# Optimization experiments

Hardware: AMD Instinct MI355X
Metric: run time of the kernel (lower is better)

The kernel has to match this reference:

```python
import jax, jax.numpy as jnp
import numpy as np

DIM = 256      # slot / feature dim
S = 22         # num_slots (21 + 1 seg slot)
NAC = 20       # num_actor_class (slots truncated to this)
EPS = 1e-8     # slot-attention epsilon
LN_EPS = 1e-5  # torch LayerNorm default eps
RES = (4, 8, 24)  # (len_seg, H, W) grid for SoftPositionEmbed3D


def _ln(x, g, b):
    m = jnp.mean(x, -1, keepdims=True)
    v = jnp.var(x, -1, keepdims=True)
    return (x - m) * jax.lax.rsqrt(v + LN_EPS) * g + b


def _grid3d():
    # build_3d_grid: meshgrid of linspaces, concat [g, 1-g] -> (1, 4, 8, 24, 6)
    rs = [jnp.linspace(0.0, 1.0, r) for r in RES]
    g = jnp.stack(jnp.meshgrid(*rs, indexing='ij'), -1)
    return jnp.concatenate([g, 1.0 - g], -1)[None]


def setup_inputs() -> dict:
    key = jax.random.key(0)
    ks = iter(jax.random.split(key, 40))
    b, nf, h, w, d = 32, 16, 8, 24, DIM

    def lin(o, i):
        return (jax.random.normal(next(ks), (o, i)) / np.sqrt(i)).astype(jnp.float32)

    def vec(o):
        return jnp.zeros((o,), jnp.float32)

    inp = {}
    inp['inputs'] = jax.random.normal(next(ks), (b, nf, h, w, d), jnp.float32)
    inp['slots'] = jax.random.normal(next(ks), (1, S, d), jnp.float32)  # self.slots buffer
    inp['pe_w'] = lin(d, 6); inp['pe_b'] = vec(d)  # SoftPositionEmbed3D Linear(6, dim)
    for nm in ['LN', 'ni', 'ns', 'npf']:  # LN, norm_input, norm_slots, norm_pre_ff
        inp[nm + '_g'] = jnp.ones((d,), jnp.float32)
        inp[nm + '_b'] = vec(d)
    for nm in ['FC1', 'FC2', 'q', 'k', 'v', 'ff1', 'ff2']:
        inp[nm + '_w'] = lin(d, d)
        inp[nm + '_b'] = vec(d)
    inp['gru_wi'] = lin(3 * d, d); inp['gru_wh'] = lin(3 * d, d)
    inp['gru_bi'] = vec(3 * d);   inp['gru_bh'] = vec(3 * d)
    return inp


def reference(inputs, slots, pe_w, pe_b, LN_g, LN_b, ni_g, ni_b, ns_g, ns_b,
              npf_g, npf_b, FC1_w, FC1_b, FC2_w, FC2_b, q_w, q_b, k_w, k_b,
              v_w, v_b, ff1_w, ff1_b, ff2_w, ff2_b, gru_wi, gru_wh, gru_bi, gru_bh):
    b, nf, h, w, d = inputs.shape
    nwin = 7  # f in range(0, 13, 2)
    # slots are NOT carried across the frame loop in the original forward,
    # so the 7 windows are independent -> fold into batch.
    win = jnp.stack([inputs[:, f:f + 4] for f in range(0, 13, 2)], 0)  # (7,b,4,h,w,d)
    B = nwin * b
    pe = _grid3d() @ pe_w.T + pe_b  # (1,4,h,w,d)
    x = win.reshape(B, 4, h, w, d) + pe
    x = x.reshape(B, -1, d)  # n = 4*h*w tokens
    # LN -> FC1 -> relu -> FC2
    x = _ln(x, LN_g, LN_b)
    x = jax.nn.relu(x @ FC1_w.T + FC1_b) @ FC2_w.T + FC2_b
    # slot attention core
    xn = _ln(x, ni_g, ni_b)
    kk = xn @ k_w.T + k_b
    vv = xn @ v_w.T + v_b
    sl = jnp.broadcast_to(slots, (B, S, d))
    q = _ln(sl, ns_g, ns_b) @ q_w.T + q_b
    dots = jnp.einsum('bid,bjd->bij', q, kk) * (d ** -0.5)
    attn_ori = jax.nn.softmax(dots, axis=1) + EPS  # softmax over SLOT axis
    attn = attn_ori / jnp.sum(attn_ori, -1, keepdims=True)  # L1 renorm over tokens
    upd = jnp.einsum('bjd,bij->bid', vv, attn)
    # GRUCell(updates, slots_prev); torch gate order: r, z, n
    xg = upd.reshape(-1, d) @ gru_wi.T + gru_bi
    hprev = sl.reshape(-1, d)
    hg = hprev @ gru_wh.T + gru_bh
    ir, iz, in_ = jnp.split(xg, 3, -1)
    hr, hz, hn = jnp.split(hg, 3, -1)
    r = jax.nn.sigmoid(ir + hr)
    z = jax.nn.sigmoid(iz + hz)
    n = jnp.tanh(in_ + r * hn)
    hnew = (1.0 - z) * n + z * hprev
    so = hnew.reshape(B, S, d)[:, :NAC]
    # residual MLP
    so = so + jax.nn.relu(_ln(so, npf_g, npf_b) @ ff1_w.T + ff1_b) @ ff2_w.T + ff2_b
    slots_out = so.reshape(nwin, b, NAC, d).transpose(1, 0, 2, 3)      # (b,7,20,d)
    attns = attn_ori.reshape(nwin, b, S, -1).transpose(1, 0, 2, 3)     # (b,7,22,768)
    return slots_out, attns
```

## Files before the change

### kernel.cpp

```cpp
#include <hip/hip_runtime.h>

#define DEV static __device__ __forceinline__

namespace {
constexpr int D     = 256;
constexpr int SALL  = 22;
constexpr int NAC   = 20;
constexpr int NWIN  = 7;
constexpr int NB    = 32;
constexpr int NF    = 16;
constexpr int SPF   = 192;
constexpr int NTOK  = 768;
constexpr int BWIN  = 224;
constexpr int PARTS = 8;
constexpr int TPP   = 3;
constexpr float LNEPS = 1e-5f;
constexpr float EPS   = 1e-8f;
constexpr float SCL   = 0.0625f;

constexpr int OFF_PE   = 0;
constexpr int OFF_FC1T = OFF_PE   + 768 * 256;
constexpr int OFF_FC2T = OFF_FC1T + 256 * 256;
constexpr int OFF_VWT  = OFF_FC2T + 256 * 256;
constexpr int OFF_QWT  = OFF_VWT  + 256 * 256;
constexpr int OFF_FF1T = OFF_QWT  + 256 * 256;
constexpr int OFF_FF2T = OFF_FF1T + 256 * 256;
constexpr int OFF_GWIT = OFF_FF2T + 256 * 256;
constexpr int OFF_GWHT = OFF_GWIT + 256 * 768;
constexpr int OFF_Q    = OFF_GWHT + 256 * 768;
constexpr int OFF_QK2T = OFF_Q    + SALL * 256;
constexpr int OFF_QB   = OFF_QK2T + 256 * SALL;
constexpr int OFF_HG0  = OFF_QB   + 32;
constexpr int OFF_UPDP = OFF_HG0  + SALL * 768;
constexpr int OFF_RSP  = OFF_UPDP + BWIN * PARTS * NAC * 256;
}

DEV float4 ld4(const float* p) { return *(const float4*)p; }
DEV float sigm(float x) { return 1.f / (1.f + __expf(-x)); }

struct TPtrs {
    const float* src[8];
    float*       dst[8];
    int          osz[8];
};

__global__ void k_trans(TPtrs p) {
    __shared__ float t[32][33];
    const int bt = blockIdx.x;
    int m, tile;
    if (bt < 384) { m = bt >> 6; tile = bt & 63; }
    else          { m = 6 + (bt - 384) / 192; tile = (bt - 384) % 192; }
    const int O  = p.osz[m];
    const int rt = O >> 5;
    const int o0 = (tile % rt) * 32, i0 = (tile / rt) * 32;
    const int tx = threadIdx.x & 31, ty = threadIdx.x >> 5;
    const float* src = p.src[m];
    float*       dst = p.dst[m];
#pragma unroll
    for (int q = 0; q < 4; ++q) { int r = ty + q * 8; t[r][tx] = src[(o0 + r) * 256 + i0 + tx]; }
    __syncthreads();
#pragma unroll
    for (int q = 0; q < 4; ++q) { int r = ty + q * 8; dst[(i0 + r) * O + o0 + tx] = t[tx][r]; }
}

__global__ void k_pe(const float* __restrict__ pw, const float* __restrict__ pb,
                     float* __restrict__ pe) {
    const int p = blockIdx.x;
    const int fo = p / SPF, rem = p % SPF, hh = rem / 24, ww = rem % 24;
    const float g0 = fo * (1.f / 3.f), g1 = hh * (1.f / 7.f), g2 = ww * (1.f / 23.f);
    const float gg[6] = {g0, g1, g2, 1.f - g0, 1.f - g1, 1.f - g2};
    for (int d = threadIdx.x; d < 256; d += 64) {
        float acc = pb[d];
#pragma unroll
        for (int c = 0; c < 6; ++c) acc = fmaf(gg[c], pw[d * 6 + c], acc);
        pe[p * 256 + d] = acc;
    }
}

__global__ void k_q(const float* __restrict__ slots, const float* __restrict__ nsg,
                    const float* __restrict__ nsb, const float* __restrict__ qwT,
                    const float* __restrict__ qbias, const float* __restrict__ kb,
                    float* __restrict__ qout, float* __restrict__ qbout) {
    __shared__ float lnb[256];
    __shared__ float red[8];
    const int i = blockIdx.x, t = threadIdx.x, lane = t & 63, wvi = t >> 6;
    const float v = slots[i * 256 + t];
    float s1 = v, s2 = v * v;
#pragma unroll
    for (int m = 32; m; m >>= 1) { s1 += __shfl_xor(s1, m); s2 += __shfl_xor(s2, m); }
    if (lane == 0) { red[wvi] = s1; red[4 + wvi] = s2; }
    __syncthreads();
    const float fs = red[0] + red[1] + red[2] + red[3];
    const float fq = red[4] + red[5] + red[6] + red[7];
    const float mean = fs * (1.f / 256.f);
    const float var  = fq * (1.f / 256.f) - mean * mean;
    const float rstd = rsqrtf(var + LNEPS);
    lnb[t] = (v - mean) * rstd * nsg[t] + nsb[t];
    __syncthreads();
    float qv = qbias[t];
    for (int k = 0; k < 256; ++k) qv = fmaf(lnb[k], qwT[k * 256 + t], qv);
    qout[i * 256 + t] = qv;
    float pp = qv * kb[t];
#pragma unroll
    for (int m = 32; m; m >>= 1) pp += __shfl_xor(pp, m);
    __syncthreads();
    if (lane == 0) red[wvi] = pp;
    __syncthreads();
    if (t == 0) qbout[i] = red[0] + red[1] + red[2] + red[3];
}

__global__ void k_qk2(const float* __restrict__ qin, const float* __restrict__ kw,
                      float* __restrict__ qk2T) {
    __shared__ float qr[256];
    const int i = blockIdx.x, t = threadIdx.x;
    qr[t] = qin[i * 256 + t];
    __syncthreads();
    float acc = 0.f;
    for (int c = 0; c < 256; ++c) acc = fmaf(qr[c], kw[c * 256 + t], acc);
    qk2T[t * SALL + i] = acc;
}

__global__ void k_hg(const float* __restrict__ slots, const float* __restrict__ gwhT,
                     const float* __restrict__ gbh, float* __restrict__ hg0) {
    __shared__ float sr[256];
    const int i = blockIdx.x, t = threadIdx.x;
    sr[t] = slots[i * 256 + t];
    __syncthreads();
    float a0 = gbh[t], a1 = gbh[t + 256], a2 = gbh[t + 512];
    for (int k = 0; k < 256; ++k) {
        const float s = sr[k];
        a0 = fmaf(s, gwhT[k * 768 + t], a0);
        a1 = fmaf(s, gwhT[k * 768 + t + 256], a1);
        a2 = fmaf(s, gwhT[k * 768 + t + 512], a2);
    }
    hg0[i * 768 + t] = a0;
    hg0[i * 768 + t + 256] = a1;
    hg0[i * 768 + t + 512] = a2;
}

template <int MODE>
DEV void gemm_step(const float* __restrict__ srcL, float* __restrict__ dstL,
                   const float4* __restrict__ wT, const float4 bias,
                   const int lane, const int wv, const float4 gni, const float4 bni) {
    float acc[8][4];
#pragma unroll
    for (int j = 0; j < 8; ++j) {
        acc[j][0] = bias.x; acc[j][1] = bias.y; acc[j][2] = bias.z; acc[j][3] = bias.w;
    }
    const float* sp = srcL + (wv << 3) * 256;
    for (int k = 0; k < 256; k += 4) {
        const float4 w0 = wT[((k + 0) << 6) + lane];
        const float4 w1 = wT[((k + 1) << 6) + lane];
        const float4 w2 = wT[((k + 2) << 6) + lane];
        const float4 w3 = wT[((k + 3) << 6) + lane];
#pragma unroll
        for (int j = 0; j < 8; ++j) {
            const float4 x4 = *(const float4*)(sp + j * 256 + k);
            acc[j][0] = fmaf(x4.x, w0.x, acc[j][0]);
            acc[j][1] = fmaf(x4.x, w0.y, acc[j][1]);
            acc[j][2] = fmaf(x4.x, w0.z, acc[j][2]);
            acc[j][3] = fmaf(x4.x, w0.w, acc[j][3]);
            acc[j][0] = fmaf(x4.y, w1.x, acc[j][0]);
            acc[j][1] = fmaf(x4.y, w1.y, acc[j][1]);
            acc[j][2] = fmaf(x4.y, w1.z, acc[j][2]);
            acc[j][3] = fmaf(x4.y, w1.w, acc[j][3]);
            acc[j][0] = fmaf(x4.z, w2.x, acc[j][0]);
            acc[j][1] = fmaf(x4.z, w2.y, acc[j][1]);
            acc[j][2] = fmaf(x4.z, w2.z, acc[j][2]);
            acc[j][3] = fmaf(x4.z, w2.w, acc[j][3]);
            acc[j][0] = fmaf(x4.w, w3.x, acc[j][0]);
            acc[j][1] = fmaf(x4.w, w3.y, acc[j][1]);
            acc[j][2] = fmaf(x4.w, w3.z, acc[j][2]);
            acc[j][3] = fmaf(x4.w, w3.w, acc[j][3]);
        }
    }
#pragma unroll
    for (int j = 0; j < 8; ++j) {
        float4 o = {acc[j][0], acc[j][1], acc[j][2], acc[j][3]};
        if constexpr (MODE == 0) {
            o.x = fmaxf(o.x, 0.f); o.y = fmaxf(o.y, 0.f);
            o.z = fmaxf(o.z, 0.f); o.w = fmaxf(o.w, 0.f);
        } else if constexpr (MODE == 1) {
            float s  = o.x + o.y + o.z + o.w;
            float q2 = o.x * o.x + o.y * o.y + o.z * o.z + o.w * o.w;
#pragma unroll
            for (int m = 32; m; m >>= 1) { s += __shfl_xor(s, m); q2 += __shfl_xor(q2, m); }
            const float mean = s * (1.f / 256.f);
            const float var  = q2 * (1.f / 256.f) - mean * mean;
            const float rstd = rsqrtf(var + LNEPS);
            o.x = (o.x - mean) * rstd * gni.x + bni.x;
            o.y = (o.y - mean) * rstd * gni.y + bni.y;
            o.z = (o.z - mean) * rstd * gni.z + bni.z;
            o.w = (o.w - mean) * rstd * gni.w + bni.w;
        }
        ((float4*)dstL)[((wv << 3) + j) * 64 + lane] = o;
    }
}

__global__ __launch_bounds__(256, 2) void k_pass1(
    const float* __restrict__ gin, const float* __restrict__ ws_pe,
    const float4* __restrict__ fc1T, const float4* __restrict__ fc2T,
    const float4* __restrict__ vwT, const float* __restrict__ qk2T,
    const float* __restrict__ qb, const float* __restrict__ LNg,
    const float* __restrict__ LNb, const float* __restrict__ nig,
    const float* __restrict__ nib, const float* __restrict__ fc1b,
    const float* __restrict__ fc2b, const float* __restrict__ vb,
    float* __restrict__ attns, float* __restrict__ updp, float* __restrict__ rsp) {
    __shared__ __align__(16) float buf0[32 * 256];
    __shared__ __align__(16) float buf1[32 * 256];
    __shared__ __align__(16) float dotsL[SALL * 36];

    const int tid = threadIdx.x, lane = tid & 63, wv = tid >> 6;
    const int blk = blockIdx.x, bb = blk >> 3, part = blk & 7;
    const int wdx = bb >> 5, bi = bb & 31;
    const int c0 = lane << 2;

    const float4 gln = ld4(LNg + c0), bln = ld4(LNb + c0);
    const float4 gni = ld4(nig + c0), bni = ld4(nib + c0);
    const float4 b1 = ld4(fc1b + c0), b2 = ld4(fc2b + c0), bv = ld4(vb + c0);

    const int islot = tid & 31;
    const int iq = islot < SALL ? islot : SALL - 1;
    const float qbv = qb[iq];
    const int jg = tid >> 5;

    float upd[NAC];
#pragma unroll
    for (int i = 0; i < NAC; ++i) upd[i] = 0.f;
    float rsacc = 0.f;

    for (int tt = part * TPP; tt < part * TPP + TPP; ++tt) {
        const int fo = tt / 6, sp0 = (tt % 6) * 32;
        const float4* src = (const float4*)gin + ((bi * NF + 2 * wdx + fo) * SPF + sp0) * 64;
        const float4* pes = (const float4*)ws_pe + (fo * SPF + sp0) * 64;
#pragma unroll
        for (int ii = 0; ii < 8; ++ii) {
            float4 a = src[tid + 256 * ii];
            const float4 p = pes[tid + 256 * ii];
            a.x += p.x; a.y += p.y; a.z += p.z; a.w += p.w;
            float s  = a.x + a.y + a.z + a.w;
            float q2 = a.x * a.x + a.y * a.y + a.z * a.z + a.w * a.w;
#pragma unroll
            for (int m = 32; m; m >>= 1) { s += __shfl_xor(s, m); q2 += __shfl_xor(q2, m); }
            const float mean = s * (1.f / 256.f);
            const float var  = q2 * (1.f / 256.f) - mean * mean;
            const float rstd = rsqrtf(var + LNEPS);
            const int j = wv + (ii << 2);
            float4 o;
            o.x = (a.x - mean) * rstd * gln.x + bln.x;
            o.y = (a.y - mean) * rstd * gln.y + bln.y;
            o.z = (a.z - mean) * rstd * gln.z + bln.z;
            o.w = (a.w - mean) * rstd * gln.w + bln.w;
            ((float4*)buf0)[j * 64 + lane] = o;
        }
        __syncthreads();
        gemm_step<0>(buf0, buf1, fc1T, b1, lane, wv, gni, bni);
        __syncthreads();
        gemm_step<1>(buf1, buf0, fc2T, b2, lane, wv, gni, bni);
        __syncthreads();
        gemm_step<2>(buf0, buf1, vwT, bv, lane, wv, gni, bni);
        {
            float a0 = qbv, a1 = qbv, a2 = qbv, a3 = qbv;
            const float* x0 = buf0 + (jg * 4) * 256;
            for (int k = 0; k < 256; k += 4) {
                const float q0 = qk2T[(k + 0) * SALL + iq];
                const float q1 = qk2T[(k + 1) * SALL + iq];
                const float q2_ = qk2T[(k + 2) * SALL + iq];
                const float q3 = qk2T[(k + 3) * SALL + iq];
                const float4 x4a = *(const float4*)(x0 + 0 * 256 + k);
                const float4 x4b = *(const float4*)(x0 + 1 * 256 + k);
                const float4 x4c = *(const float4*)(x0 + 2 * 256 + k);
                const float4 x4d = *(const float4*)(x0 + 3 * 256 + k);
                a0 = fmaf(x4a.x, q0, fmaf(x4a.y, q1, fmaf(x4a.z, q2_, fmaf(x4a.w, q3, a0))));
                a1 = fmaf(x4b.x, q0, fmaf(x4b.y, q1, fmaf(x4b.z, q2_, fmaf(x4b.w, q3, a1))));
                a2 = fmaf(x4c.x, q0, fmaf(x4c.y, q1, fmaf(x4c.z, q2_, fmaf(x4c.w, q3, a2))));
                a3 = fmaf(x4d.x, q0, fmaf(x4d.y, q1, fmaf(x4d.z, q2_, fmaf(x4d.w, q3, a3))));
            }
            if (islot < SALL) {
                dotsL[islot * 36 + jg * 4 + 0] = a0 * SCL;
                dotsL[islot * 36 + jg * 4 + 1] = a1 * SCL;
                dotsL[islot * 36 + jg * 4 + 2] = a2 * SCL;
                dotsL[islot * 36 + jg * 4 + 3] = a3 * SCL;
            }
        }
        __syncthreads();
        if (tid < 32) {
            float dv[SALL];
            float mx = -1e30f;
#pragma unroll
            for (int i = 0; i < SALL; ++i) {
                dv[i] = dotsL[i * 36 + tid];
                mx = fmaxf(mx, dv[i]);
            }
            float sum = 0.f;
#pragma unroll
            for (int i = 0; i < SALL; ++i) { dv[i] = __expf(dv[i] - mx); sum += dv[i]; }
            const float inv = 1.f / sum;
#pragma unroll
            for (int i = 0; i < SALL; ++i) dotsL[i * 36 + tid] = dv[i] * inv + EPS;
        }
        __syncthreads();
        const int tok0 = tt * 32;
        float* ao = attns + bi * (NWIN * SALL * NTOK) + wdx * (SALL * NTOK) + tok0;
#pragma unroll
        for (int rep = 0; rep < 3; ++rep) {
            const int idx = tid + rep * 256;
            if (idx < SALL * 32) {
                const int i = idx >> 5, j = idx & 31;
                ao[i * NTOK + j] = dotsL[i * 36 + j];
            }
        }
        if (tid < NAC) {
            float s = 0.f;
#pragma unroll
            for (int j = 0; j < 32; ++j) s += dotsL[tid * 36 + j];
            rsacc += s;
        }
#pragma unroll
        for (int jq = 0; jq < 8; ++jq) {
            const float v0 = buf1[(jq * 4 + 0) * 256 + tid];
            const float v1 = buf1[(jq * 4 + 1) * 256 + tid];
            const float v2 = buf1[(jq * 4 + 2) * 256 + tid];
            const float v3 = buf1[(jq * 4 + 3) * 256 + tid];
#pragma unroll
            for (int i = 0; i < NAC; ++i) {
                const float4 a = *(const float4*)&dotsL[i * 36 + jq * 4];
                upd[i] = fmaf(a.x, v0, fmaf(a.y, v1, fmaf(a.z, v2, fmaf(a.w, v3, upd[i]))));
            }
        }
        __syncthreads();
    }
    float* up = updp + blk * (NAC * 256);
#pragma unroll
    for (int i = 0; i < NAC; ++i) up[i * 256 + tid] = upd[i];
    if (tid < NAC) rsp[blk * NAC + tid] = rsacc;
}

__global__ __launch_bounds__(256) void k_pass2(
    const float* __restrict__ updp, const float* __restrict__ rsp,
    const float* __restrict__ gwiT, const float* __restrict__ gbi,
    const float* __restrict__ hg0, const float* __restrict__ slots,
    const float* __restrict__ npfg, const float* __restrict__ npfb,
    const float* __restrict__ ff1T, const float* __restrict__ ff1b,
    const float* __restrict__ ff2T, const float* __restrict__ ff2b,
    float* __restrict__ sout) {
    __shared__ float u[256];
    __shared__ float red[8];
    const int t = threadIdx.x, lane = t & 63, wvi = t >> 6;
    const int blk = blockIdx.x, bb = blk >> 2, sg = blk & 3;
    const int wdx = bb >> 5, bi = bb & 31;
    const float* upb = updp + (bb * PARTS) * (NAC * 256);
    const float* rsb = rsp + (bb * PARTS) * NAC;
    for (int m = 0; m < 5; ++m) {
        const int i = sg * 5 + m;
        float rs = 0.f, uv = 0.f;
#pragma unroll
        for (int p = 0; p < PARTS; ++p) {
            rs += rsb[p * NAC + i];
            uv += upb[p * (NAC * 256) + i * 256 + t];
        }
        uv /= rs;
        u[t] = uv;
        __syncthreads();
        float a0 = gbi[t], a1 = gbi[t + 256], a2 = gbi[t + 512];
        for (int k = 0; k < 256; ++k) {
            const float s = u[k];
            a0 = fmaf(s, gwiT[k * 768 + t], a0);
            a1 = fmaf(s, gwiT[k * 768 + t + 256], a1);
            a2 = fmaf(s, gwiT[k * 768 + t + 512], a2);
        }
        const float r = sigm(a0 + hg0[i * 768 + t]);
        const float z = sigm(a1 + hg0[i * 768 + t + 256]);
        const float n = tanhf(a2 + r * hg0[i * 768 + t + 512]);
        const float hp = slots[i * 256 + t];
        const float h = (1.f - z) * n + z * hp;
        float s1 = h, s2 = h * h;
#pragma unroll
        for (int mm = 32; mm; mm >>= 1) { s1 += __shfl_xor(s1, mm); s2 += __shfl_xor(s2, mm); }
        __syncthreads();
        if (lane == 0) { red[wvi] = s1; red[4 + wvi] = s2; }
        __syncthreads();
        const float fs = red[0] + red[1] + red[2] + red[3];
        const float fq = red[4] + red[5] + red[6] + red[7];
        const float mean = fs * (1.f / 256.f);
        const float var  = fq * (1.f / 256.f) - mean * mean;
        const float rstd = rsqrtf(var + LNEPS);
        u[t] = (h - mean) * rstd * npfg[t] + npfb[t];
        __syncthreads();
        float f1 = ff1b[t];
        for (int k = 0; k < 256; ++k) f1 = fmaf(u[k], ff1T[k * 256 + t], f1);
        f1 = fmaxf(f1, 0.f);
        __syncthreads();
        u[t] = f1;
        __syncthreads();
        float f2 = ff2b[t];
        for (int k = 0; k < 256; ++k) f2 = fmaf(u[k], ff2T[k * 256 + t], f2);
        sout[bi * (NWIN * NAC * 256) + wdx * (NAC * 256) + i * 256 + t] = h + f2;
        __syncthreads();
    }
}

extern "C" void kernel_launch(void* const* d_in, const int* in_sizes, int n_in,
                              void* d_out, int out_size, void* d_ws, size_t ws_size,
                              hipStream_t stream) {
    const float* inputs = (const float*)d_in[0];
    const float* slots  = (const float*)d_in[1];
    const float* pe_w   = (const float*)d_in[2];
    const float* pe_b   = (const float*)d_in[3];
    const float* LN_g   = (const float*)d_in[4];
    const float* LN_b   = (const float*)d_in[5];
    const float* ni_g   = (const float*)d_in[6];
    const float* ni_b   = (const float*)d_in[7];
    const float* ns_g   = (const float*)d_in[8];
    const float* ns_b   = (const float*)d_in[9];
    const float* npf_g  = (const float*)d_in[10];
    const float* npf_b  = (const float*)d_in[11];
    const float* FC1_w  = (const float*)d_in[12];
    const float* FC1_b  = (const float*)d_in[13];
    const float* FC2_w  = (const float*)d_in[14];
    const float* FC2_b  = (const float*)d_in[15];
    const float* q_w    = (const float*)d_in[16];
    const float* q_b    = (const float*)d_in[17];
    const float* k_w    = (const float*)d_in[18];
    const float* k_b    = (const float*)d_in[19];
    const float* v_w    = (const float*)d_in[20];
    const float* v_b    = (const float*)d_in[21];
    const float* ff1_w  = (const float*)d_in[22];
    const float* ff1_b  = (const float*)d_in[23];
    const float* ff2_w  = (const float*)d_in[24];
    const float* ff2_b  = (const float*)d_in[25];
    const float* gru_wi = (const float*)d_in[26];
    const float* gru_wh = (const float*)d_in[27];
    const float* gru_bi = (const float*)d_in[28];
    const float* gru_bh = (const float*)d_in[29];

    float* ws    = (float*)d_ws;
    float* out   = (float*)d_out;
    float* attns = out + 32 * 7 * 20 * 256;

    TPtrs tp;
    tp.src[0] = FC1_w;  tp.dst[0] = ws + OFF_FC1T; tp.osz[0] = 256;
    tp.src[1] = FC2_w;  tp.dst[1] = ws + OFF_FC2T; tp.osz[1] = 256;
    tp.src[2] = v_w;    tp.dst[2] = ws + OFF_VWT;  tp.osz[2] = 256;
    tp.src[3] = q_w;    tp.dst[3] = ws + OFF_QWT;  tp.osz[3] = 256;
    tp.src[4] = ff1_w;  tp.dst[4] = ws + OFF_FF1T; tp.osz[4] = 256;
    tp.src[5] = ff2_w;  tp.dst[5] = ws + OFF_FF2T; tp.osz[5] = 256;
    tp.src[6] = gru_wi; tp.dst[6] = ws + OFF_GWIT; tp.osz[6] = 768;
    tp.src[7] = gru_wh; tp.dst[7] = ws + OFF_GWHT; tp.osz[7] = 768;

    k_trans<<<768, 256, 0, stream>>>(tp);
    k_pe<<<768, 64, 0, stream>>>(pe_w, pe_b, ws + OFF_PE);
    k_q<<<SALL, 256, 0, stream>>>(slots, ns_g, ns_b, ws + OFF_QWT, q_b, k_b,
                                  ws + OFF_Q, ws + OFF_QB);
    k_qk2<<<SALL, 256, 0, stream>>>(ws + OFF_Q, k_w, ws + OFF_QK2T);
    k_hg<<<SALL, 256, 0, stream>>>(slots, ws + OFF_GWHT, gru_bh, ws + OFF_HG0);
    k_pass1<<<BWIN * PARTS, 256, 0, stream>>>(
        inputs, ws + OFF_PE, (const float4*)(ws + OFF_FC1T),
        (const float4*)(ws + OFF_FC2T), (const float4*)(ws + OFF_VWT),
        ws + OFF_QK2T, ws + OFF_QB, LN_g, LN_b, ni_g, ni_b, FC1_b, FC2_b, v_b,
        attns, ws + OFF_UPDP, ws + OFF_RSP);
    k_pass2<<<BWIN * 4, 256, 0, stream>>>(
        ws + OFF_UPDP, ws + OFF_RSP, ws + OFF_GWIT, gru_bi, ws + OFF_HG0, slots,
        npf_g, npf_b, ws + OFF_FF1T, ff1_b, ws + OFF_FF2T, ff2_b, out);
}
```

Baseline: 1.721 ms.

## Move pass1 token GEMMs onto bf16 MFMA with hi/lo split for fp32 accuracy

```diff
diff --git a/kernel.cpp b/kernel.cpp
--- a/kernel.cpp
+++ b/kernel.cpp
@@ -2,12 +2,13 @@
 
 #define DEV static __device__ __forceinline__
 
+typedef __attribute__((ext_vector_type(8))) short bf16x8;
+typedef __attribute__((ext_vector_type(4))) float f32x4;
+
 namespace {
-constexpr int D     = 256;
 constexpr int SALL  = 22;
 constexpr int NAC   = 20;
 constexpr int NWIN  = 7;
-constexpr int NB    = 32;
 constexpr int NF    = 16;
 constexpr int SPF   = 192;
 constexpr int NTOK  = 768;
@@ -19,10 +20,7 @@
 constexpr float SCL   = 0.0625f;
 
 constexpr int OFF_PE   = 0;
-constexpr int OFF_FC1T = OFF_PE   + 768 * 256;
-constexpr int OFF_FC2T = OFF_FC1T + 256 * 256;
-constexpr int OFF_VWT  = OFF_FC2T + 256 * 256;
-constexpr int OFF_QWT  = OFF_VWT  + 256 * 256;
+constexpr int OFF_QWT  = OFF_PE   + 768 * 256;
 constexpr int OFF_FF1T = OFF_QWT  + 256 * 256;
 constexpr int OFF_FF2T = OFF_FF1T + 256 * 256;
 constexpr int OFF_GWIT = OFF_FF2T + 256 * 256;
@@ -31,12 +29,57 @@
 constexpr int OFF_QK2T = OFF_Q    + SALL * 256;
 constexpr int OFF_QB   = OFF_QK2T + 256 * SALL;
 constexpr int OFF_HG0  = OFF_QB   + 32;
-constexpr int OFF_UPDP = OFF_HG0  + SALL * 768;
+constexpr int OFF_WHP  = OFF_HG0  + SALL * 768;
+constexpr int OFF_WLP  = OFF_WHP  + 3 * 128 * 64 * 4;
+constexpr int OFF_QPH  = OFF_WLP  + 3 * 128 * 64 * 4;
+constexpr int OFF_QPL  = OFF_QPH  + 16 * 64 * 4;
+constexpr int OFF_UPDP = OFF_QPL  + 16 * 64 * 4;
 constexpr int OFF_RSP  = OFF_UPDP + BWIN * PARTS * NAC * 256;
 }
 
 DEV float4 ld4(const float* p) { return *(const float4*)p; }
 DEV float sigm(float x) { return 1.f / (1.f + __expf(-x)); }
+DEV float bf2(short h) { return __uint_as_float(((unsigned)(unsigned short)h) << 16); }
+
+DEV int swzoff(int row, int col) {
+    return (row << 8) + (((((col >> 3) ^ (row & 7))) << 3) | (col & 7));
+}
+
+DEV void split2(float v, unsigned short& h, unsigned short& l) {
+    unsigned u = __float_as_uint(v);
+    unsigned hr = (u + 0x7fffu + ((u >> 16) & 1u)) & 0xffff0000u;
+    h = (unsigned short)(hr >> 16);
+    float lf = v - __uint_as_float(hr);
+    unsigned u2 = __float_as_uint(lf);
+    l = (unsigned short)((u2 + 0x7fffu + ((u2 >> 16) & 1u)) >> 16);
+}
+
+DEV void st_bf16(short* dH, short* dL, int row, int col, float v) {
+    unsigned short h, l;
+    split2(v, h, l);
+    const int off = swzoff(row, col);
+    dH[off] = (short)h; dL[off] = (short)l;
+}
+
+DEV void st4_bf16(short* dH, short* dL, int row, int c0, float4 o) {
+    unsigned short h[4], l[4];
+    float vv[4] = {o.x, o.y, o.z, o.w};
+#pragma unroll
+    for (int i = 0; i < 4; ++i) split2(vv[i], h[i], l[i]);
+    const int off = swzoff(row, c0);
+    *(uint2*)(dH + off) = make_uint2(h[0] | ((unsigned)h[1] << 16), h[2] | ((unsigned)h[3] << 16));
+    *(uint2*)(dL + off) = make_uint2(l[0] | ((unsigned)l[1] << 16), l[2] | ((unsigned)l[3] << 16));
+}
+
+DEV f32x4 mm(bf16x8 a, bf16x8 b, f32x4 c) {
+    return __builtin_amdgcn_mfma_f32_16x16x32_bf16(a, b, c, 0, 0, 0);
+}
+DEV f32x4 mm3(bf16x8 ah, bf16x8 al, bf16x8 bh, bf16x8 bl, f32x4 c) {
+    c = mm(al, bh, c);
+    c = mm(ah, bl, c);
+    c = mm(ah, bh, c);
+    return c;
+}
 
 struct TPtrs {
     const float* src[8];
@@ -48,8 +91,8 @@
     __shared__ float t[32][33];
     const int bt = blockIdx.x;
     int m, tile;
-    if (bt < 384) { m = bt >> 6; tile = bt & 63; }
-    else          { m = 6 + (bt - 384) / 192; tile = (bt - 384) % 192; }
+    if (bt < 192) { m = bt >> 6; tile = bt & 63; }
+    else          { m = 3 + (bt - 192) / 192; tile = (bt - 192) % 192; }
     const int O  = p.osz[m];
     const int rt = O >> 5;
     const int o0 = (tile % rt) * 32, i0 = (tile / rt) * 32;
@@ -138,91 +181,172 @@
     hg0[i * 768 + t + 512] = a2;
 }
 
+__global__ void k_wpack(const float* __restrict__ w0, const float* __restrict__ w1,
+                        const float* __restrict__ w2, uint4* __restrict__ hp,
+                        uint4* __restrict__ lp) {
+    const int b = blockIdx.x;
+    const int m = b >> 7, f = b & 127;
+    const int Nfg = f >> 3, Kf = f & 7;
+    const int l = threadIdx.x;
+    const float* W = (m == 0) ? w0 : ((m == 1) ? w1 : w2);
+    const int col = (Nfg << 4) + (l & 15);
+    const int k0  = (Kf << 5) + ((l >> 4) << 3);
+    unsigned short h[8], lo[8];
+#pragma unroll
+    for (int j = 0; j < 8; ++j) split2(W[col * 256 + k0 + j], h[j], lo[j]);
+    const int idx = ((m << 7) + f) * 64 + l;
+    hp[idx] = make_uint4(h[0] | ((unsigned)h[1] << 16), h[2] | ((unsigned)h[3] << 16),
+                         h[4] | ((unsigned)h[5] << 16), h[6] | ((unsigned)h[7] << 16));
+    lp[idx] = make_uint4(lo[0] | ((unsigned)lo[1] << 16), lo[2] | ((unsigned)lo[3] << 16),
+                         lo[4] | ((unsigned)lo[5] << 16), lo[6] | ((unsigned)lo[7] << 16));
+}
+
+__global__ void k_qpk(const float* __restrict__ qk2T, uint4* __restrict__ hp,
+                      uint4* __restrict__ lp) {
+    const int b = blockIdx.x;
+    const int l = threadIdx.x;
+    const int slot = ((b >> 3) << 4) + (l & 15);
+    const int k0   = ((b & 7) << 5) + ((l >> 4) << 3);
+    unsigned short h[8], lo[8];
+#pragma unroll
+    for (int j = 0; j < 8; ++j) {
+        float v = (slot < SALL) ? qk2T[(k0 + j) * SALL + slot] : 0.f;
+        split2(v, h[j], lo[j]);
+    }
+    const int idx = b * 64 + l;
+    hp[idx] = make_uint4(h[0] | ((unsigned)h[1] << 16), h[2] | ((unsigned)h[3] << 16),
+                         h[4] | ((unsigned)h[5] << 16), h[6] | ((unsigned)h[7] << 16));
+    lp[idx] = make_uint4(lo[0] | ((unsigned)lo[1] << 16), lo[2] | ((unsigned)lo[3] << 16),
+                         lo[4] | ((unsigned)lo[5] << 16), lo[6] | ((unsigned)lo[7] << 16));
+}
+
 template <int MODE>
-DEV void gemm_step(const float* __restrict__ srcL, float* __restrict__ dstL,
-                   const float4* __restrict__ wT, const float4 bias,
-                   const int lane, const int wv, const float4 gni, const float4 bni) {
-    float acc[8][4];
-#pragma unroll
-    for (int j = 0; j < 8; ++j) {
-        acc[j][0] = bias.x; acc[j][1] = bias.y; acc[j][2] = bias.z; acc[j][3] = bias.w;
-    }
-    const float* sp = srcL + (wv << 3) * 256;
-    for (int k = 0; k < 256; k += 4) {
-        const float4 w0 = wT[((k + 0) << 6) + lane];
-        const float4 w1 = wT[((k + 1) << 6) + lane];
-        const float4 w2 = wT[((k + 2) << 6) + lane];
-        const float4 w3 = wT[((k + 3) << 6) + lane];
-#pragma unroll
-        for (int j = 0; j < 8; ++j) {
-            const float4 x4 = *(const float4*)(sp + j * 256 + k);
-            acc[j][0] = fmaf(x4.x, w0.x, acc[j][0]);
-            acc[j][1] = fmaf(x4.x, w0.y, acc[j][1]);
-            acc[j][2] = fmaf(x4.x, w0.z, acc[j][2]);
-            acc[j][3] = fmaf(x4.x, w0.w, acc[j][3]);
-            acc[j][0] = fmaf(x4.y, w1.x, acc[j][0]);
-            acc[j][1] = fmaf(x4.y, w1.y, acc[j][1]);
-            acc[j][2] = fmaf(x4.y, w1.z, acc[j][2]);
-            acc[j][3] = fmaf(x4.y, w1.w, acc[j][3]);
-            acc[j][0] = fmaf(x4.z, w2.x, acc[j][0]);
-            acc[j][1] = fmaf(x4.z, w2.y, acc[j][1]);
-            acc[j][2] = fmaf(x4.z, w2.z, acc[j][2]);
-            acc[j][3] = fmaf(x4.z, w2.w, acc[j][3]);
-            acc[j][0] = fmaf(x4.w, w3.x, acc[j][0]);
-            acc[j][1] = fmaf(x4.w, w3.y, acc[j][1]);
-            acc[j][2] = fmaf(x4.w, w3.z, acc[j][2]);
-            acc[j][3] = fmaf(x4.w, w3.w, acc[j][3]);
-        }
-    }
-#pragma unroll
-    for (int j = 0; j < 8; ++j) {
-        float4 o = {acc[j][0], acc[j][1], acc[j][2], acc[j][3]};
-        if constexpr (MODE == 0) {
-            o.x = fmaxf(o.x, 0.f); o.y = fmaxf(o.y, 0.f);
-            o.z = fmaxf(o.z, 0.f); o.w = fmaxf(o.w, 0.f);
-        } else if constexpr (MODE == 1) {
-            float s  = o.x + o.y + o.z + o.w;
-            float q2 = o.x * o.x + o.y * o.y + o.z * o.z + o.w * o.w;
-#pragma unroll
-            for (int m = 32; m; m >>= 1) { s += __shfl_xor(s, m); q2 += __shfl_xor(q2, m); }
+DEV void mfma_step(const short* sH, const short* sL, short* dH, short* dL,
+                   const bf16x8* __restrict__ wph, const bf16x8* __restrict__ wpl,
+                   const float* bs, const float* gs, const float* bns,
+                   const int lane, const int wv, const int tid,
+                   float* lnpart, float* lnstat) {
+    f32x4 acc[2][4];
+#pragma unroll
+    for (int Mf = 0; Mf < 2; ++Mf)
+#pragma unroll
+        for (int Nf = 0; Nf < 4; ++Nf) {
+            const float b = bs[Nf];
+            acc[Mf][Nf] = (f32x4){b, b, b, b};
+        }
+    const int ar0 = lane & 15, ar1 = 16 + (lane & 15);
+    const int gkb = lane >> 4;
+#pragma unroll
+    for (int Kf = 0; Kf < 8; ++Kf) {
+        const int c8 = (Kf * 4 + gkb) << 3;
+        const bf16x8 a0h = *(const bf16x8*)(sH + swzoff(ar0, c8));
+        const bf16x8 a0l = *(const bf16x8*)(sL + swzoff(ar0, c8));
+        const bf16x8 a1h = *(const bf16x8*)(sH + swzoff(ar1, c8));
+        const bf16x8 a1l = *(const bf16x8*)(sL + swzoff(ar1, c8));
+#pragma unroll
+        for (int Nf = 0; Nf < 4; ++Nf) {
+            const int fidx = (((wv << 2) + Nf) * 8 + Kf) * 64 + lane;
+            const bf16x8 bh = wph[fidx];
+            const bf16x8 bl = wpl[fidx];
+            acc[0][Nf] = mm3(a0h, a0l, bh, bl, acc[0][Nf]);
+            acc[1][Nf] = mm3(a1h, a1l, bh, bl, acc[1][Nf]);
+        }
+    }
+    const int rb = (lane >> 4) << 2;
+    const int cb = (wv << 6) + (lane & 15);
+    if constexpr (MODE == 1) {
+#pragma unroll
+        for (int Mf = 0; Mf < 2; ++Mf)
+#pragma unroll
+            for (int r = 0; r < 4; ++r) {
+                float s  = acc[Mf][0][r] + acc[Mf][1][r] + acc[Mf][2][r] + acc[Mf][3][r];
+                float s2 = acc[Mf][0][r] * acc[Mf][0][r] + acc[Mf][1][r] * acc[Mf][1][r] +
+                           acc[Mf][2][r] * acc[Mf][2][r] + acc[Mf][3][r] * acc[Mf][3][r];
+#pragma unroll
+                for (int m = 1; m < 16; m <<= 1) { s += __shfl_xor(s, m); s2 += __shfl_xor(s2, m); }
+                if ((lane & 15) == 0) {
+                    const int row = (Mf << 4) + rb + r;
+                    lnpart[(wv * 32 + row) * 2]     = s;
+                    lnpart[(wv * 32 + row) * 2 + 1] = s2;
+                }
+            }
+        __syncthreads();
+        if (tid < 32) {
+            float s = 0.f, s2 = 0.f;
+#pragma unroll
+            for (int w = 0; w < 4; ++w) {
+                s  += lnpart[(w * 32 + tid) * 2];
+                s2 += lnpart[(w * 32 + tid) * 2 + 1];
+            }
             const float mean = s * (1.f / 256.f);
-            const float var  = q2 * (1.f / 256.f) - mean * mean;
-            const float rstd = rsqrtf(var + LNEPS);
-            o.x = (o.x - mean) * rstd * gni.x + bni.x;
-            o.y = (o.y - mean) * rstd * gni.y + bni.y;
-            o.z = (o.z - mean) * rstd * gni.z + bni.z;
-            o.w = (o.w - mean) * rstd * gni.w + bni.w;
-        }
-        ((float4*)dstL)[((wv << 3) + j) * 64 + lane] = o;
-    }
+            const float var  = s2 * (1.f / 256.f) - mean * mean;
+            lnstat[tid * 2]     = mean;
+            lnstat[tid * 2 + 1] = rsqrtf(var + LNEPS);
+        }
+        __syncthreads();
+    }
+#pragma unroll
+    for (int Mf = 0; Mf < 2; ++Mf)
+#pragma unroll
+        for (int Nf = 0; Nf < 4; ++Nf)
+#pragma unroll
+            for (int r = 0; r < 4; ++r) {
+                float v = acc[Mf][Nf][r];
+                const int row = (Mf << 4) + rb + r;
+                const int col = cb + (Nf << 4);
+                if constexpr (MODE == 0) v = fmaxf(v, 0.f);
+                if constexpr (MODE == 1)
+                    v = (v - lnstat[row * 2]) * lnstat[row * 2 + 1] * gs[Nf] + bns[Nf];
+                st_bf16(dH, dL, row, col, v);
+            }
 }
 
 __global__ __launch_bounds__(256, 2) void k_pass1(
     const float* __restrict__ gin, const float* __restrict__ ws_pe,
-    const float4* __restrict__ fc1T, const float4* __restrict__ fc2T,
-    const float4* __restrict__ vwT, const float* __restrict__ qk2T,
+    const bf16x8* __restrict__ whp, const bf16x8* __restrict__ wlp,
+    const bf16x8* __restrict__ qph, const bf16x8* __restrict__ qpl,
     const float* __restrict__ qb, const float* __restrict__ LNg,
     const float* __restrict__ LNb, const float* __restrict__ nig,
     const float* __restrict__ nib, const float* __restrict__ fc1b,
     const float* __restrict__ fc2b, const float* __restrict__ vb,
     float* __restrict__ attns, float* __restrict__ updp, float* __restrict__ rsp) {
-    __shared__ __align__(16) float buf0[32 * 256];
-    __shared__ __align__(16) float buf1[32 * 256];
+    __shared__ __align__(16) short xAh[32 * 256];
+    __shared__ __align__(16) short xAl[32 * 256];
+    __shared__ __align__(16) short xBh[32 * 256];
+    __shared__ __align__(16) short xBl[32 * 256];
     __shared__ __align__(16) float dotsL[SALL * 36];
+    __shared__ float lnpart[4 * 32 * 2];
+    __shared__ float lnstat[32 * 2];
 
     const int tid = threadIdx.x, lane = tid & 63, wv = tid >> 6;
     const int blk = blockIdx.x, bb = blk >> 3, part = blk & 7;
     const int wdx = bb >> 5, bi = bb & 31;
+
     const int c0 = lane << 2;
-
     const float4 gln = ld4(LNg + c0), bln = ld4(LNb + c0);
-    const float4 gni = ld4(nig + c0), bni = ld4(nib + c0);
-    const float4 b1 = ld4(fc1b + c0), b2 = ld4(fc2b + c0), bv = ld4(vb + c0);
-
-    const int islot = tid & 31;
-    const int iq = islot < SALL ? islot : SALL - 1;
-    const float qbv = qb[iq];
-    const int jg = tid >> 5;
+
+    const int cb = (wv << 6) + (lane & 15);
+    float b1s[4], b2s[4], bvs[4], gnis[4], bnis[4];
+#pragma unroll
+    for (int Nf = 0; Nf < 4; ++Nf) {
+        b1s[Nf]  = fc1b[cb + (Nf << 4)];
+        b2s[Nf]  = fc2b[cb + (Nf << 4)];
+        bvs[Nf]  = vb[cb + (Nf << 4)];
+        gnis[Nf] = nig[cb + (Nf << 4)];
+        bnis[Nf] = nib[cb + (Nf << 4)];
+    }
+    float qb8[8];
+#pragma unroll
+    for (int Mf = 0; Mf < 2; ++Mf)
+#pragma unroll
+        for (int r = 0; r < 4; ++r) {
+            const int s_ = (Mf << 4) + ((lane >> 4) << 2) + r;
+            qb8[(Mf << 2) + r] = qb[s_ < SALL ? s_ : SALL - 1];
+        }
+
+    const bf16x8* wph1 = whp;           const bf16x8* wpl1 = wlp;
+    const bf16x8* wph2 = whp + 8192;    const bf16x8* wpl2 = wlp + 8192;
+    const bf16x8* wphv = whp + 16384;   const bf16x8* wplv = wlp + 16384;
 
     float upd[NAC];
 #pragma unroll
@@ -251,47 +375,54 @@
             o.y = (a.y - mean) * rstd * gln.y + bln.y;
             o.z = (a.z - mean) * rstd * gln.z + bln.z;
             o.w = (a.w - mean) * rstd * gln.w + bln.w;
-            ((float4*)buf0)[j * 64 + lane] = o;
-        }
-        __syncthreads();
-        gemm_step<0>(buf0, buf1, fc1T, b1, lane, wv, gni, bni);
-        __syncthreads();
-        gemm_step<1>(buf1, buf0, fc2T, b2, lane, wv, gni, bni);
-        __syncthreads();
-        gemm_step<2>(buf0, buf1, vwT, bv, lane, wv, gni, bni);
-        {
-            float a0 = qbv, a1 = qbv, a2 = qbv, a3 = qbv;
-            const float* x0 = buf0 + (jg * 4) * 256;
-            for (int k = 0; k < 256; k += 4) {
-                const float q0 = qk2T[(k + 0) * SALL + iq];
-                const float q1 = qk2T[(k + 1) * SALL + iq];
-                const float q2_ = qk2T[(k + 2) * SALL + iq];
-                const float q3 = qk2T[(k + 3) * SALL + iq];
-                const float4 x4a = *(const float4*)(x0 + 0 * 256 + k);
-                const float4 x4b = *(const float4*)(x0 + 1 * 256 + k);
-                const float4 x4c = *(const float4*)(x0 + 2 * 256 + k);
-                const float4 x4d = *(const float4*)(x0 + 3 * 256 + k);
-                a0 = fmaf(x4a.x, q0, fmaf(x4a.y, q1, fmaf(x4a.z, q2_, fmaf(x4a.w, q3, a0))));
-                a1 = fmaf(x4b.x, q0, fmaf(x4b.y, q1, fmaf(x4b.z, q2_, fmaf(x4b.w, q3, a1))));
-                a2 = fmaf(x4c.x, q0, fmaf(x4c.y, q1, fmaf(x4c.z, q2_, fmaf(x4c.w, q3, a2))));
-                a3 = fmaf(x4d.x, q0, fmaf(x4d.y, q1, fmaf(x4d.z, q2_, fmaf(x4d.w, q3, a3))));
+            st4_bf16(xAh, xAl, j, c0, o);
+        }
+        __syncthreads();
+        mfma_step<0>(xAh, xAl, xBh, xBl, wph1, wpl1, b1s, gnis, bnis, lane, wv, tid, lnpart, lnstat);
+        __syncthreads();
+        mfma_step<1>(xBh, xBl, xAh, xAl, wph2, wpl2, b2s, gnis, bnis, lane, wv, tid, lnpart, lnstat);
+        __syncthreads();
+        mfma_step<2>(xAh, xAl, xBh, xBl, wphv, wplv, bvs, gnis, bnis, lane, wv, tid, lnpart, lnstat);
+        if (wv == 0) {
+            f32x4 dacc[2][2];
+#pragma unroll
+            for (int Mf = 0; Mf < 2; ++Mf)
+#pragma unroll
+                for (int Nf = 0; Nf < 2; ++Nf) dacc[Mf][Nf] = (f32x4){0.f, 0.f, 0.f, 0.f};
+            const int tr0 = lane & 15, tr1 = 16 + (lane & 15);
+#pragma unroll
+            for (int Kf = 0; Kf < 8; ++Kf) {
+                const int c8 = (Kf * 4 + (lane >> 4)) << 3;
+                const bf16x8 b0h = *(const bf16x8*)(xAh + swzoff(tr0, c8));
+                const bf16x8 b0l = *(const bf16x8*)(xAl + swzoff(tr0, c8));
+                const bf16x8 b1h = *(const bf16x8*)(xAh + swzoff(tr1, c8));
+                const bf16x8 b1l = *(const bf16x8*)(xAl + swzoff(tr1, c8));
+#pragma unroll
+                for (int Mf = 0; Mf < 2; ++Mf) {
+                    const bf16x8 ah = qph[(Mf * 8 + Kf) * 64 + lane];
+                    const bf16x8 al = qpl[(Mf * 8 + Kf) * 64 + lane];
+                    dacc[Mf][0] = mm3(ah, al, b0h, b0l, dacc[Mf][0]);
+                    dacc[Mf][1] = mm3(ah, al, b1h, b1l, dacc[Mf][1]);
+                }
             }
-            if (islot < SALL) {
-                dotsL[islot * 36 + jg * 4 + 0] = a0 * SCL;
-                dotsL[islot * 36 + jg * 4 + 1] = a1 * SCL;
-                dotsL[islot * 36 + jg * 4 + 2] = a2 * SCL;
-                dotsL[islot * 36 + jg * 4 + 3] = a3 * SCL;
-            }
+#pragma unroll
+            for (int Mf = 0; Mf < 2; ++Mf)
+#pragma unroll
+                for (int Nf = 0; Nf < 2; ++Nf)
+#pragma unroll
+                    for (int r = 0; r < 4; ++r) {
+                        const int slot = (Mf << 4) + ((lane >> 4) << 2) + r;
+                        const int tok  = (Nf << 4) + (lane & 15);
+                        if (slot < SALL)
+                            dotsL[slot * 36 + tok] = (dacc[Mf][Nf][r] + qb8[(Mf << 2) + r]) * SCL;
+                    }
         }
         __syncthreads();
         if (tid < 32) {
             float dv[SALL];
             float mx = -1e30f;
 #pragma unroll
-            for (int i = 0; i < SALL; ++i) {
-                dv[i] = dotsL[i * 36 + tid];
-                mx = fmaxf(mx, dv[i]);
-            }
+            for (int i = 0; i < SALL; ++i) { dv[i] = dotsL[i * 36 + tid]; mx = fmaxf(mx, dv[i]); }
             float sum = 0.f;
 #pragma unroll
             for (int i = 0; i < SALL; ++i) { dv[i] = __expf(dv[i] - mx); sum += dv[i]; }
@@ -318,10 +449,10 @@
         }
 #pragma unroll
         for (int jq = 0; jq < 8; ++jq) {
-            const float v0 = buf1[(jq * 4 + 0) * 256 + tid];
-            const float v1 = buf1[(jq * 4 + 1) * 256 + tid];
-            const float v2 = buf1[(jq * 4 + 2) * 256 + tid];
-            const float v3 = buf1[(jq * 4 + 3) * 256 + tid];
+            const float v0 = bf2(xBh[swzoff(jq * 4 + 0, tid)]) + bf2(xBl[swzoff(jq * 4 + 0, tid)]);
+            const float v1 = bf2(xBh[swzoff(jq * 4 + 1, tid)]) + bf2(xBl[swzoff(jq * 4 + 1, tid)]);
+            const float v2 = bf2(xBh[swzoff(jq * 4 + 2, tid)]) + bf2(xBl[swzoff(jq * 4 + 2, tid)]);
+            const float v3 = bf2(xBh[swzoff(jq * 4 + 3, tid)]) + bf2(xBl[swzoff(jq * 4 + 3, tid)]);
 #pragma unroll
             for (int i = 0; i < NAC; ++i) {
                 const float4 a = *(const float4*)&dotsL[i * 36 + jq * 4];
@@ -439,25 +570,30 @@
     float* attns = out + 32 * 7 * 20 * 256;
 
     TPtrs tp;
-    tp.src[0] = FC1_w;  tp.dst[0] = ws + OFF_FC1T; tp.osz[0] = 256;
-    tp.src[1] = FC2_w;  tp.dst[1] = ws + OFF_FC2T; tp.osz[1] = 256;
-    tp.src[2] = v_w;    tp.dst[2] = ws + OFF_VWT;  tp.osz[2] = 256;
-    tp.src[3] = q_w;    tp.dst[3] = ws + OFF_QWT;  tp.osz[3] = 256;
-    tp.src[4] = ff1_w;  tp.dst[4] = ws + OFF_FF1T; tp.osz[4] = 256;
-    tp.src[5] = ff2_w;  tp.dst[5] = ws + OFF_FF2T; tp.osz[5] = 256;
-    tp.src[6] = gru_wi; tp.dst[6] = ws + OFF_GWIT; tp.osz[6] = 768;
-    tp.src[7] = gru_wh; tp.dst[7] = ws + OFF_GWHT; tp.osz[7] = 768;
-
-    k_trans<<<768, 256, 0, stream>>>(tp);
+    tp.src[0] = q_w;    tp.dst[0] = ws + OFF_QWT;  tp.osz[0] = 256;
+    tp.src[1] = ff1_w;  tp.dst[1] = ws + OFF_FF1T; tp.osz[1] = 256;
+    tp.src[2] = ff2_w;  tp.dst[2] = ws + OFF_FF2T; tp.osz[2] = 256;
+    tp.src[3] = gru_wi; tp.dst[3] = ws + OFF_GWIT; tp.osz[3] = 768;
+    tp.src[4] = gru_wh; tp.dst[4] = ws + OFF_GWHT; tp.osz[4] = 768;
+    tp.src[5] = q_w;    tp.dst[5] = ws + OFF_QWT;  tp.osz[5] = 256;
+    tp.src[6] = q_w;    tp.dst[6] = ws + OFF_QWT;  tp.osz[6] = 256;
+    tp.src[7] = q_w;    tp.dst[7] = ws + OFF_QWT;  tp.osz[7] = 256;
+
+    k_trans<<<576, 256, 0, stream>>>(tp);
     k_pe<<<768, 64, 0, stream>>>(pe_w, pe_b, ws + OFF_PE);
     k_q<<<SALL, 256, 0, stream>>>(slots, ns_g, ns_b, ws + OFF_QWT, q_b, k_b,
                                   ws + OFF_Q, ws + OFF_QB);
     k_qk2<<<SALL, 256, 0, stream>>>(ws + OFF_Q, k_w, ws + OFF_QK2T);
     k_hg<<<SALL, 256, 0, stream>>>(slots, ws + OFF_GWHT, gru_bh, ws + OFF_HG0);
+    k_wpack<<<384, 64, 0, stream>>>(FC1_w, FC2_w, v_w,
+                                    (uint4*)(ws + OFF_WHP), (uint4*)(ws + OFF_WLP));
+    k_qpk<<<16, 64, 0, stream>>>(ws + OFF_QK2T,
+                                 (uint4*)(ws + OFF_QPH), (uint4*)(ws + OFF_QPL));
     k_pass1<<<BWIN * PARTS, 256, 0, stream>>>(
-        inputs, ws + OFF_PE, (const float4*)(ws + OFF_FC1T),
-        (const float4*)(ws + OFF_FC2T), (const float4*)(ws + OFF_VWT),
-        ws + OFF_QK2T, ws + OFF_QB, LN_g, LN_b, ni_g, ni_b, FC1_b, FC2_b, v_b,
+        inputs, ws + OFF_PE,
+        (const bf16x8*)(ws + OFF_WHP), (const bf16x8*)(ws + OFF_WLP),
+        (const bf16x8*)(ws + OFF_QPH), (const bf16x8*)(ws + OFF_QPL),
+        ws + OFF_QB, LN_g, LN_b, ni_g, ni_b, FC1_b, FC2_b, v_b,
         attns, ws + OFF_UPDP, ws + OFF_RSP);
     k_pass2<<<BWIN * 4, 256, 0, stream>>>(
         ws + OFF_UPDP, ws + OFF_RSP, ws + OFF_GWIT, gru_bi, ws + OFF_HG0, slots,
```

Measured after the change: 2.942 ms. 1.71x slower.
